# Optimization experiments

Measured on AMD Instinct MI355X. Metric: run time of the kernel, lower is better.

Reference implementation:

```python
import jax, jax.numpy as jnp
import numpy as np

NUM_CHANNEL_TYPES = 32  # global channel vocabulary (matches fill_max of channel_idx)


def setup_inputs() -> dict:
    key = jax.random.key(0)
    k1, k2, k3, k4, k5, k6 = jax.random.split(key, 6)
    B, C, H, W, E, P = 32, 8, 224, 224, 768, 16
    return {
        "x": jax.random.normal(k1, (B, C, H, W), dtype=jnp.float32),
        "channel_idx": jax.random.randint(k2, (B, C), 0, NUM_CHANNEL_TYPES, dtype=jnp.int64),
        "proj_w": jax.random.normal(k3, (E, P, P), dtype=jnp.float32) * 0.02,
        "proj_b": jax.random.normal(k4, (E,), dtype=jnp.float32) * 0.02,
        "ctx_w": jax.random.normal(k5, (E, E), dtype=jnp.float32) * 0.02,
        "ctx_b": jax.random.normal(k6, (E,), dtype=jnp.float32) * 0.02,
    }


def reference(x, channel_idx, proj_w, proj_b, ctx_w, ctx_b):
    B, C, H, W = x.shape
    E, P, _ = proj_w.shape
    Hp, Wp = H // P, W // P

    # Conv3d(1, E, kernel=(1,P,P), stride=(1,P,P)) == per-channel 2D patchify matmul
    xp = x.reshape(B, C, Hp, P, Wp, P)
    emb = jnp.einsum('bchpwq,epq->bechw', xp, proj_w) + proj_b[None, :, None, None, None]
    # emb: (B, E, C, Hp, Wp)

    # per-(sample, channel) average patch embedding -> (B, C, E)
    av_patch = emb.mean(axis=(3, 4)).transpose(0, 2, 1)
    flat = av_patch.reshape(B * C, E)
    seg = channel_idx.reshape(-1)

    # segment-mean over the batch by channel index (fused scatter-mean)
    sums = jax.ops.segment_sum(flat, seg, num_segments=NUM_CHANNEL_TYPES)
    cnt = jax.ops.segment_sum(jnp.ones((B * C,), flat.dtype), seg, num_segments=NUM_CHANNEL_TYPES)
    means = sums / jnp.maximum(cnt, 1.0)[:, None]
    chan_embed = means[seg].reshape(B, C, E)  # torch computes this under no_grad

    # context projection and broadcast-add back onto patch embeddings
    ctx = chan_embed @ ctx_w.T + ctx_b            # (B, C, E)
    out = emb + ctx.transpose(0, 2, 1)[:, :, :, None, None]

    # flatten(2).transpose(1, 2): (B, C*Hp*Wp, E)
    return out.reshape(B, E, C * Hp * Wp).transpose(0, 2, 1)
```

## Files before the change

kernel.cpp:

```cpp
#include <hip/hip_runtime.h>
#include <hip/hip_bf16.h>

typedef __attribute__((ext_vector_type(8))) short s16x8;
typedef __attribute__((ext_vector_type(4))) float f32x4;
typedef __attribute__((ext_vector_type(8))) unsigned short u16x8;
typedef __attribute__((ext_vector_type(4))) unsigned short u16x4;

static __device__ __forceinline__ unsigned short f2bf(float f) {
  unsigned int u = __float_as_uint(f);
  unsigned int r = u + 0x7fffu + ((u >> 16) & 1u);
  return (unsigned short)(r >> 16);
}
static __device__ __forceinline__ float bf2f(unsigned short s) {
  return __uint_as_float(((unsigned int)s) << 16);
}

static __device__ __forceinline__ void gload16(const void* g, void* l) {
  __builtin_amdgcn_global_load_lds(
      (const __attribute__((address_space(1))) unsigned int*)g,
      (__attribute__((address_space(3))) unsigned int*)l, 16, 0, 0);
}


__global__ void k_cvt(const float* __restrict__ in, unsigned short* __restrict__ o) {
  int i = blockIdx.x * 256 + threadIdx.x;
  float4 v = reinterpret_cast<const float4*>(in)[i];
  u16x4 pk = { f2bf(v.x), f2bf(v.y), f2bf(v.z), f2bf(v.w) };
  reinterpret_cast<u16x4*>(o)[i] = pk;
}

__global__ void k_transpose768(const float* __restrict__ in, float* __restrict__ out) {
  __shared__ float tile[32][33];
  int bx = blockIdx.x % 24, by = blockIdx.x / 24;
  int tx = threadIdx.x & 31, ty = threadIdx.x >> 5;
#pragma unroll
  for (int k = 0; k < 4; ++k)
    tile[ty + 8 * k][tx] = in[(size_t)(by * 32 + ty + 8 * k) * 768 + bx * 32 + tx];
  __syncthreads();
#pragma unroll
  for (int k = 0; k < 4; ++k)
    out[(size_t)(bx * 32 + ty + 8 * k) * 768 + by * 32 + tx] = tile[tx][ty + 8 * k];
}

__global__ __launch_bounds__(256) void k_prep(const float* __restrict__ x,
                                              unsigned short* __restrict__ xbf,
                                              float* __restrict__ avg3) {
  __shared__ __align__(16) unsigned short strip[14 * 256];
  int b = blockIdx.x;
  int bc = b / 14, hp = b - bc * 14;
  int t = threadIdx.x;
  const float* img = x + ((size_t)bc * 224 + hp * 16) * 224;

  for (int idx = t; idx < 896; idx += 256) {
    int row = idx / 56, c4 = idx - row * 56;
    float4 v = reinterpret_cast<const float4*>(img + (size_t)row * 224)[c4];
    int wp = c4 >> 2, q0 = (c4 & 3) << 2;
    u16x4 pk = { f2bf(v.x), f2bf(v.y), f2bf(v.z), f2bf(v.w) };
    *(u16x4*)&strip[wp * 256 + row * 16 + q0] = pk;
  }
  __syncthreads();

  float acc = 0.f;
#pragma unroll
  for (int wp = 0; wp < 14; ++wp) acc += bf2f(strip[wp * 256 + t]);
  avg3[((size_t)bc * 14 + hp) * 256 + t] = acc;

  const u16x8* so = (const u16x8*)strip;
  u16x8* go = (u16x8*)(xbf + ((size_t)bc * 196 + hp * 14) * 256);
  for (int i = t; i < 448; i += 256) go[i] = so[i];
}

__global__ __launch_bounds__(256) void k_segmean(const float* __restrict__ avg3,
                                                 const int* __restrict__ seg,
                                                 float* __restrict__ sp) {
  __shared__ float red[4][64];
  __shared__ int rcnt[4];
  __shared__ int ssg[256];
  int s = blockIdx.x & 31, kc = blockIdx.x >> 5;
  int t = threadIdx.x;
  int kl = t & 63, slice = t >> 6;
  int k = kc * 64 + kl;
  ssg[t] = seg[t];
  __syncthreads();
  float sum = 0.f; int cnt = 0;
  for (int bc = slice * 64; bc < slice * 64 + 64; ++bc) {
    if (ssg[bc] == s) {
      ++cnt;
      const float* row = avg3 + (size_t)bc * 14 * 256 + k;
#pragma unroll
      for (int hp = 0; hp < 14; ++hp) sum += row[hp * 256];
    }
  }
  red[slice][kl] = sum;
  if (kl == 0) rcnt[slice] = cnt;
  __syncthreads();
  if (t < 64) {
    float tot = red[0][t] + red[1][t] + red[2][t] + red[3][t];
    int c = rcnt[0] + rcnt[1] + rcnt[2] + rcnt[3];
    sp[s * 256 + kc * 64 + t] = tot / (196.0f * (float)(c > 0 ? c : 1));
  }
}

__global__ __launch_bounds__(256) void k_means2(const float* __restrict__ sp,
                                                const float* __restrict__ pw,
                                                const float* __restrict__ pb,
                                                float* __restrict__ means) {
  __shared__ float ssp[256];
  __shared__ float red[8][32];
  int s = blockIdx.x & 31, e0 = (blockIdx.x >> 5) << 5;
  int t = threadIdx.x;
  int e = t & 31, ksl = t >> 5;
  ssp[t] = sp[s * 256 + t];
  __syncthreads();
  const float4* w = reinterpret_cast<const float4*>(pw + (size_t)(e0 + e) * 256 + ksl * 32);
  float a = 0.f;
#pragma unroll
  for (int j = 0; j < 8; ++j) {
    float4 v = w[j];
    int kb = ksl * 32 + j * 4;
    a += v.x * ssp[kb] + v.y * ssp[kb + 1] + v.z * ssp[kb + 2] + v.w * ssp[kb + 3];
  }
  red[ksl][e] = a;
  __syncthreads();
  if (t < 32) {
    float tot = 0.f;
#pragma unroll
    for (int j = 0; j < 8; ++j) tot += red[j][t];
    means[s * 768 + e0 + t] = tot + pb[e0 + t];
  }
}

__global__ __launch_bounds__(256) void k_ctx2(const float* __restrict__ means,
                                              const float* __restrict__ cwT,
                                              const float* __restrict__ cb,
                                              const float* __restrict__ pb,
                                              float* __restrict__ addv) {
  __shared__ float mn[768];
  __shared__ float red[8][32];
  int s = blockIdx.x & 31, e0 = (blockIdx.x >> 5) << 5;
  int t = threadIdx.x;
  int e = t & 31, fsl = t >> 5;
  mn[t] = means[s * 768 + t];
  mn[t + 256] = means[s * 768 + 256 + t];
  mn[t + 512] = means[s * 768 + 512 + t];
  __syncthreads();
  const float* col = cwT + (size_t)fsl * 96 * 768 + e0 + e;
  float a = 0.f;
#pragma unroll 8
  for (int j = 0; j < 96; ++j) a += mn[fsl * 96 + j] * col[(size_t)j * 768];
  red[fsl][e] = a;
  __syncthreads();
  if (t < 32) {
    float tot = 0.f;
#pragma unroll
    for (int j = 0; j < 8; ++j) tot += red[j][t];
    addv[s * 768 + e0 + t] = tot + cb[e0 + t] + pb[e0 + t];
  }
}

__global__ __launch_bounds__(256) void k_gemm(
    const unsigned short* __restrict__ xbf, const unsigned short* __restrict__ wbf,
    const float* __restrict__ addv, const int* __restrict__ seg,
    float* __restrict__ out) {
  __shared__ __align__(16) unsigned short Al[128 * 64];
  __shared__ __align__(16) unsigned short Bl[128 * 64];

  int bid = blockIdx.x;
  int xcd = bid & 7, local = bid >> 3;
  int mb = xcd * 49 + local / 6;
  int nb = local - (local / 6) * 6;
  int m0 = mb << 7, n0 = nb << 7;

  int t = threadIdx.x;
  int wave = t >> 6, lane = t & 63;
  int wm = (wave >> 1) << 6, wn = (wave & 1) << 6;
  int lr = lane & 15, hi = lane >> 4;
  int axor = (lr & 7) << 4;

  int swz = (((lane & 7) ^ ((lane >> 3) & 7)) << 4);
  const char* abase = (const char*)xbf + (size_t)(m0 + (lane >> 3)) * 512 + swz + (size_t)wave * 16384;
  const char* bbase = (const char*)wbf + (size_t)(n0 + (lane >> 3)) * 512 + swz + (size_t)wave * 16384;
  char* adst = (char*)Al + wave * 4096;
  char* bdst = (char*)Bl + wave * 4096;
  const char* Alc = (const char*)Al;
  const char* Blc = (const char*)Bl;

  f32x4 acc[4][4] = {};

  for (int kt = 0; kt < 4; ++kt) {
#pragma unroll
    for (int i = 0; i < 4; ++i) {
      gload16(abase + kt * 128 + i * 4096, adst + i * 1024);
      gload16(bbase + kt * 128 + i * 4096, bdst + i * 1024);
    }
    __syncthreads();
#pragma unroll
    for (int kk = 0; kk < 2; ++kk) {
      s16x8 af[4], bv[4];
      int koff = kk * 64 + hi * 16;
#pragma unroll
      for (int i = 0; i < 4; ++i)
        af[i] = *(const s16x8*)(Alc + (wm + i * 16 + lr) * 128 + (koff ^ axor));
#pragma unroll
      for (int j = 0; j < 4; ++j)
        bv[j] = *(const s16x8*)(Blc + (wn + j * 16 + lr) * 128 + (koff ^ axor));
#pragma unroll
      for (int i = 0; i < 4; ++i)
#pragma unroll
        for (int j = 0; j < 4; ++j)
          acc[i][j] = __builtin_amdgcn_mfma_f32_16x16x32_bf16(af[i], bv[j], acc[i][j], 0, 0, 0);
    }
    __syncthreads();
  }

#pragma unroll
  for (int i = 0; i < 4; ++i) {
    int mloc = m0 + wm + i * 16 + (hi << 2);
#pragma unroll
    for (int r = 0; r < 4; ++r) {
      int M = mloc + r;
      int sgi = seg[M / 196];
      const float* av = addv + (size_t)sgi * 768 + n0 + wn + lr;
      float* orow = out + (size_t)M * 768 + n0 + wn + lr;
#pragma unroll
      for (int j = 0; j < 4; ++j)
        orow[j * 16] = acc[i][j][r] + av[j * 16];
    }
  }
}

__global__ void k_avgpatch_fb(const float* __restrict__ x, float* __restrict__ avg) {
  int bc = blockIdx.x;
  int k = threadIdx.x;
  int p = k >> 4, q = k & 15;
  const float* base = x + (size_t)bc * 224 * 224;
  float s = 0.f;
  for (int hp = 0; hp < 14; ++hp) {
    const float* row = base + (hp * 16 + p) * 224 + q;
#pragma unroll
    for (int wp = 0; wp < 14; ++wp) s += row[wp * 16];
  }
  avg[bc * 256 + k] = s * (1.0f / 196.0f);
}

__global__ __launch_bounds__(768) void k_chain_fb(const float* __restrict__ avg,
                                                  const int* __restrict__ seg,
                                                  const float* __restrict__ pw,
                                                  const float* __restrict__ pb,
                                                  const float* __restrict__ cwT,
                                                  const float* __restrict__ cb,
                                                  float* __restrict__ addv) {
  __shared__ float sp[256];
  __shared__ float mn[768];
  __shared__ int ssg[256];
  int s = blockIdx.x, t = threadIdx.x;
  if (t < 256) ssg[t] = seg[t];
  __syncthreads();
  if (t < 256) {
    float sum = 0.f; int c = 0;
    for (int bc = 0; bc < 256; ++bc)
      if (ssg[bc] == s) { sum += avg[bc * 256 + t]; ++c; }
    sp[t] = sum / (float)(c > 0 ? c : 1);
  }
  __syncthreads();
  {
    const float4* w = reinterpret_cast<const float4*>(pw + (size_t)t * 256);
    float a = 0.f;
#pragma unroll 8
    for (int k = 0; k < 64; ++k) {
      float4 v = w[k];
      a += v.x * sp[k * 4] + v.y * sp[k * 4 + 1] + v.z * sp[k * 4 + 2] + v.w * sp[k * 4 + 3];
    }
    mn[t] = a + pb[t];
  }
  __syncthreads();
  float a2 = 0.f;
#pragma unroll 8
  for (int f = 0; f < 768; ++f) a2 += mn[f] * cwT[(size_t)f * 768 + t];
  addv[s * 768 + t] = a2 + cb[t] + pb[t];
}

__global__ __launch_bounds__(256) void k_gemm_fb(
    const float* __restrict__ x, const unsigned short* __restrict__ wbf,
    const float* __restrict__ addv, const int* __restrict__ seg,
    float* __restrict__ out) {
  __shared__ unsigned short Al[128][40];
  __shared__ unsigned short Bl[128][40];
  int bid = blockIdx.x;
  int xcd = bid & 7, local = bid >> 3;
  int mb = xcd * 49 + local / 6;
  int nb = local - (local / 6) * 6;
  int m0 = mb << 7, n0 = nb << 7;
  int t = threadIdx.x;
  int wave = t >> 6, lane = t & 63;
  int wm = (wave >> 1) << 6, wn = (wave & 1) << 6;
  int lr = lane & 15, lk = (lane >> 4) << 3;
  int mstage = m0 + (t >> 1);
  int halfA = t & 1;
  int bc = mstage / 196;
  int pij = mstage - bc * 196;
  int hp = pij / 14;
  int wp = pij - hp * 14;
  const float* xbase = x + ((size_t)bc * 224 + hp * 16 + halfA) * 224 + wp * 16;
  const unsigned short* bsrc = wbf + (size_t)(n0 + (t >> 1)) * 256 + halfA * 16;
  unsigned short* adst = &Al[t >> 1][halfA * 16];
  unsigned short* bdst = &Bl[t >> 1][halfA * 16];
  f32x4 acc[4][4] = {};
  for (int ks = 0; ks < 8; ++ks) {
    __syncthreads();
    *(u16x8*)bdst       = *(const u16x8*)(bsrc + ks * 32);
    *(u16x8*)(bdst + 8) = *(const u16x8*)(bsrc + ks * 32 + 8);
    {
      const float4* src = reinterpret_cast<const float4*>(xbase + ks * 448);
      float4 v0 = src[0], v1 = src[1], v2 = src[2], v3 = src[3];
      u16x8 p0 = { f2bf(v0.x), f2bf(v0.y), f2bf(v0.z), f2bf(v0.w),
                   f2bf(v1.x), f2bf(v1.y), f2bf(v1.z), f2bf(v1.w) };
      u16x8 p1 = { f2bf(v2.x), f2bf(v2.y), f2bf(v2.z), f2bf(v2.w),
                   f2bf(v3.x), f2bf(v3.y), f2bf(v3.z), f2bf(v3.w) };
      *(u16x8*)adst = p0;
      *(u16x8*)(adst + 8) = p1;
    }
    __syncthreads();
    s16x8 af[4], bfv[4];
#pragma unroll
    for (int i = 0; i < 4; ++i) af[i] = *(const s16x8*)&Al[wm + i * 16 + lr][lk];
#pragma unroll
    for (int j = 0; j < 4; ++j) bfv[j] = *(const s16x8*)&Bl[wn + j * 16 + lr][lk];
#pragma unroll
    for (int i = 0; i < 4; ++i)
#pragma unroll
      for (int j = 0; j < 4; ++j)
        acc[i][j] = __builtin_amdgcn_mfma_f32_16x16x32_bf16(af[i], bfv[j], acc[i][j], 0, 0, 0);
  }
#pragma unroll
  for (int i = 0; i < 4; ++i) {
    int mloc = m0 + wm + i * 16 + ((lane >> 4) << 2);
#pragma unroll
    for (int r = 0; r < 4; ++r) {
      int M = mloc + r;
      int sgi = seg[M / 196];
      const float* av = addv + (size_t)sgi * 768 + n0 + wn + lr;
      float* orow = out + (size_t)M * 768 + n0 + wn + lr;
#pragma unroll
      for (int j = 0; j < 4; ++j)
        orow[j * 16] = acc[i][j][r] + av[j * 16];
    }
  }
}


extern "C" void kernel_launch(void* const* d_in, const int* in_sizes, int n_in,
                              void* d_out, int out_size, void* d_ws, size_t ws_size,
                              hipStream_t stream) {
  (void)in_sizes; (void)n_in; (void)out_size;
  const float* x  = (const float*)d_in[0];
  const int*   sg = (const int*)d_in[1];
  const float* pw = (const float*)d_in[2];
  const float* pb = (const float*)d_in[3];
  const float* cw = (const float*)d_in[4];
  const float* cb = (const float*)d_in[5];
  float* out = (float*)d_out;

  char* ws = (char*)d_ws;
  unsigned short* pwbf = (unsigned short*)ws;
  float* cwT   = (float*)(ws + 393216);
  float* addv  = (float*)(ws + 2752512);
  float* sp    = (float*)(ws + 2850816);
  float* means = (float*)(ws + 2883584);
  float* avg3  = (float*)(ws + 2981888);
  unsigned short* xbf = (unsigned short*)(ws + 6651904);
  const size_t NEED = 6651904u + 25690112u;

  k_cvt<<<192, 256, 0, stream>>>(pw, pwbf);
  k_transpose768<<<576, 256, 0, stream>>>(cw, cwT);
  if (ws_size >= NEED) {
    k_prep<<<3584, 256, 0, stream>>>(x, xbf, avg3);
    k_segmean<<<128, 256, 0, stream>>>(avg3, sg, sp);
    k_means2<<<768, 256, 0, stream>>>(sp, pw, pb, means);
    k_ctx2<<<768, 256, 0, stream>>>(means, cwT, cb, pb, addv);
    k_gemm<<<2352, 256, 0, stream>>>(xbf, pwbf, addv, sg, out);
  } else {
    float* avgp = (float*)(ws + 2981888);
    k_avgpatch_fb<<<256, 256, 0, stream>>>(x, avgp);
    k_chain_fb<<<32, 768, 0, stream>>>(avgp, sg, pw, pb, cwT, cb, addv);
    k_gemm_fb<<<2352, 256, 0, stream>>>(x, pwbf, addv, sg, out);
  }
}
```

Before: 101.6 us.

## Merge prep kernels into one launch and vectorize GEMM epilogue stores via swapped MFMA operands

Folds the weight bf16 conversion and the ctx_w transpose into the x-prep kernel as extra block ranges, cutting two kernel launches and their serialization. It also swaps the MFMA A/B operands so each lane holds four consecutive output columns. That lets the epilogue do 16-byte vector loads of the add vector and 16-byte stores of the output instead of scalar strided stores. The output write is the dominant memory traffic, so wider stores should improve write coalescing.

```diff
diff --git a/kernel.cpp b/kernel.cpp
--- a/kernel.cpp
+++ b/kernel.cpp
@@ -21,53 +21,52 @@
       (__attribute__((address_space(3))) unsigned int*)l, 16, 0, 0);
 }
 
-
-__global__ void k_cvt(const float* __restrict__ in, unsigned short* __restrict__ o) {
-  int i = blockIdx.x * 256 + threadIdx.x;
-  float4 v = reinterpret_cast<const float4*>(in)[i];
-  u16x4 pk = { f2bf(v.x), f2bf(v.y), f2bf(v.z), f2bf(v.w) };
-  reinterpret_cast<u16x4*>(o)[i] = pk;
-}
-
-__global__ void k_transpose768(const float* __restrict__ in, float* __restrict__ out) {
-  __shared__ float tile[32][33];
-  int bx = blockIdx.x % 24, by = blockIdx.x / 24;
-  int tx = threadIdx.x & 31, ty = threadIdx.x >> 5;
-#pragma unroll
-  for (int k = 0; k < 4; ++k)
-    tile[ty + 8 * k][tx] = in[(size_t)(by * 32 + ty + 8 * k) * 768 + bx * 32 + tx];
-  __syncthreads();
-#pragma unroll
-  for (int k = 0; k < 4; ++k)
-    out[(size_t)(bx * 32 + ty + 8 * k) * 768 + by * 32 + tx] = tile[tx][ty + 8 * k];
-}
-
-__global__ __launch_bounds__(256) void k_prep(const float* __restrict__ x,
+__global__ __launch_bounds__(256) void k_mega(const float* __restrict__ x,
                                               unsigned short* __restrict__ xbf,
-                                              float* __restrict__ avg3) {
-  __shared__ __align__(16) unsigned short strip[14 * 256];
-  int b = blockIdx.x;
-  int bc = b / 14, hp = b - bc * 14;
-  int t = threadIdx.x;
-  const float* img = x + ((size_t)bc * 224 + hp * 16) * 224;
-
-  for (int idx = t; idx < 896; idx += 256) {
-    int row = idx / 56, c4 = idx - row * 56;
-    float4 v = reinterpret_cast<const float4*>(img + (size_t)row * 224)[c4];
-    int wp = c4 >> 2, q0 = (c4 & 3) << 2;
+                                              float* __restrict__ avg3,
+                                              const float* __restrict__ pw,
+                                              unsigned short* __restrict__ pwbf,
+                                              const float* __restrict__ cw,
+                                              float* __restrict__ cwT) {
+  __shared__ __align__(16) char smem[7168];
+  int b = blockIdx.x, t = threadIdx.x;
+  if (b < 3584) {
+    unsigned short* strip = (unsigned short*)smem;
+    int bc = b / 14, hp = b - bc * 14;
+    const float* img = x + ((size_t)bc * 224 + hp * 16) * 224;
+    for (int idx = t; idx < 896; idx += 256) {
+      int row = idx / 56, c4 = idx - row * 56;
+      float4 v = reinterpret_cast<const float4*>(img + (size_t)row * 224)[c4];
+      int wp = c4 >> 2, q0 = (c4 & 3) << 2;
+      u16x4 pk = { f2bf(v.x), f2bf(v.y), f2bf(v.z), f2bf(v.w) };
+      *(u16x4*)&strip[wp * 256 + row * 16 + q0] = pk;
+    }
+    __syncthreads();
+    float acc = 0.f;
+#pragma unroll
+    for (int wp = 0; wp < 14; ++wp) acc += bf2f(strip[wp * 256 + t]);
+    avg3[((size_t)bc * 14 + hp) * 256 + t] = acc;
+    const u16x8* so = (const u16x8*)strip;
+    u16x8* go = (u16x8*)(xbf + ((size_t)bc * 196 + hp * 14) * 256);
+    for (int i = t; i < 448; i += 256) go[i] = so[i];
+  } else if (b < 3776) {
+    int i = (b - 3584) * 256 + t;
+    float4 v = reinterpret_cast<const float4*>(pw)[i];
     u16x4 pk = { f2bf(v.x), f2bf(v.y), f2bf(v.z), f2bf(v.w) };
-    *(u16x4*)&strip[wp * 256 + row * 16 + q0] = pk;
-  }
-  __syncthreads();
-
-  float acc = 0.f;
-#pragma unroll
-  for (int wp = 0; wp < 14; ++wp) acc += bf2f(strip[wp * 256 + t]);
-  avg3[((size_t)bc * 14 + hp) * 256 + t] = acc;
-
-  const u16x8* so = (const u16x8*)strip;
-  u16x8* go = (u16x8*)(xbf + ((size_t)bc * 196 + hp * 14) * 256);
-  for (int i = t; i < 448; i += 256) go[i] = so[i];
+    reinterpret_cast<u16x4*>(pwbf)[i] = pk;
+  } else {
+    float (*tile)[33] = (float(*)[33])smem;
+    int bid2 = b - 3776;
+    int bx = bid2 % 24, by = bid2 / 24;
+    int tx = t & 31, ty = t >> 5;
+#pragma unroll
+    for (int k = 0; k < 4; ++k)
+      tile[ty + 8 * k][tx] = cw[(size_t)(by * 32 + ty + 8 * k) * 768 + bx * 32 + tx];
+    __syncthreads();
+#pragma unroll
+    for (int k = 0; k < 4; ++k)
+      cwT[(size_t)(bx * 32 + ty + 8 * k) * 768 + by * 32 + tx] = tile[tx][ty + 8 * k];
+  }
 }
 
 __global__ __launch_bounds__(256) void k_segmean(const float* __restrict__ avg3,
@@ -208,25 +207,45 @@
       for (int i = 0; i < 4; ++i)
 #pragma unroll
         for (int j = 0; j < 4; ++j)
-          acc[i][j] = __builtin_amdgcn_mfma_f32_16x16x32_bf16(af[i], bv[j], acc[i][j], 0, 0, 0);
+          acc[i][j] = __builtin_amdgcn_mfma_f32_16x16x32_bf16(bv[j], af[i], acc[i][j], 0, 0, 0);
     }
     __syncthreads();
   }
 
 #pragma unroll
   for (int i = 0; i < 4; ++i) {
-    int mloc = m0 + wm + i * 16 + (hi << 2);
-#pragma unroll
-    for (int r = 0; r < 4; ++r) {
-      int M = mloc + r;
-      int sgi = seg[M / 196];
-      const float* av = addv + (size_t)sgi * 768 + n0 + wn + lr;
-      float* orow = out + (size_t)M * 768 + n0 + wn + lr;
-#pragma unroll
-      for (int j = 0; j < 4; ++j)
-        orow[j * 16] = acc[i][j][r] + av[j * 16];
-    }
-  }
+    int M = m0 + wm + i * 16 + lr;
+    int sgi = seg[M / 196];
+    const float* av = addv + (size_t)sgi * 768 + n0 + wn + hi * 4;
+    float* orow = out + (size_t)M * 768 + n0 + wn + hi * 4;
+#pragma unroll
+    for (int j = 0; j < 4; ++j) {
+      f32x4 a4 = *(const f32x4*)(av + j * 16);
+      f32x4 v = acc[i][j];
+      v.x += a4.x; v.y += a4.y; v.z += a4.z; v.w += a4.w;
+      *(f32x4*)(orow + j * 16) = v;
+    }
+  }
+}
+
+__global__ void k_cvt_fb(const float* __restrict__ in, unsigned short* __restrict__ o) {
+  int i = blockIdx.x * 256 + threadIdx.x;
+  float4 v = reinterpret_cast<const float4*>(in)[i];
+  u16x4 pk = { f2bf(v.x), f2bf(v.y), f2bf(v.z), f2bf(v.w) };
+  reinterpret_cast<u16x4*>(o)[i] = pk;
+}
+
+__global__ void k_transpose_fb(const float* __restrict__ in, float* __restrict__ out) {
+  __shared__ float tile[32][33];
+  int bx = blockIdx.x % 24, by = blockIdx.x / 24;
+  int tx = threadIdx.x & 31, ty = threadIdx.x >> 5;
+#pragma unroll
+  for (int k = 0; k < 4; ++k)
+    tile[ty + 8 * k][tx] = in[(size_t)(by * 32 + ty + 8 * k) * 768 + bx * 32 + tx];
+  __syncthreads();
+#pragma unroll
+  for (int k = 0; k < 4; ++k)
+    out[(size_t)(bx * 32 + ty + 8 * k) * 768 + by * 32 + tx] = tile[tx][ty + 8 * k];
 }
 
 __global__ void k_avgpatch_fb(const float* __restrict__ x, float* __restrict__ avg) {
@@ -330,20 +349,21 @@
     for (int i = 0; i < 4; ++i)
 #pragma unroll
       for (int j = 0; j < 4; ++j)
-        acc[i][j] = __builtin_amdgcn_mfma_f32_16x16x32_bf16(af[i], bfv[j], acc[i][j], 0, 0, 0);
+        acc[i][j] = __builtin_amdgcn_mfma_f32_16x16x32_bf16(bfv[j], af[i], acc[i][j], 0, 0, 0);
   }
 #pragma unroll
   for (int i = 0; i < 4; ++i) {
-    int mloc = m0 + wm + i * 16 + ((lane >> 4) << 2);
-#pragma unroll
-    for (int r = 0; r < 4; ++r) {
-      int M = mloc + r;
-      int sgi = seg[M / 196];
-      const float* av = addv + (size_t)sgi * 768 + n0 + wn + lr;
-      float* orow = out + (size_t)M * 768 + n0 + wn + lr;
-#pragma unroll
-      for (int j = 0; j < 4; ++j)
-        orow[j * 16] = acc[i][j][r] + av[j * 16];
+    int M = m0 + wm + i * 16 + lr;
+    int sgi = seg[M / 196];
+    int hi = lane >> 4;
+    const float* av = addv + (size_t)sgi * 768 + n0 + wn + hi * 4;
+    float* orow = out + (size_t)M * 768 + n0 + wn + hi * 4;
+#pragma unroll
+    for (int j = 0; j < 4; ++j) {
+      f32x4 a4 = *(const f32x4*)(av + j * 16);
+      f32x4 v = acc[i][j];
+      v.x += a4.x; v.y += a4.y; v.z += a4.z; v.w += a4.w;
+      *(f32x4*)(orow + j * 16) = v;
     }
   }
 }
@@ -371,16 +391,16 @@
   unsigned short* xbf = (unsigned short*)(ws + 6651904);
   const size_t NEED = 6651904u + 25690112u;
 
-  k_cvt<<<192, 256, 0, stream>>>(pw, pwbf);
-  k_transpose768<<<576, 256, 0, stream>>>(cw, cwT);
   if (ws_size >= NEED) {
-    k_prep<<<3584, 256, 0, stream>>>(x, xbf, avg3);
+    k_mega<<<4352, 256, 0, stream>>>(x, xbf, avg3, pw, pwbf, cw, cwT);
     k_segmean<<<128, 256, 0, stream>>>(avg3, sg, sp);
     k_means2<<<768, 256, 0, stream>>>(sp, pw, pb, means);
     k_ctx2<<<768, 256, 0, stream>>>(means, cwT, cb, pb, addv);
     k_gemm<<<2352, 256, 0, stream>>>(xbf, pwbf, addv, sg, out);
   } else {
     float* avgp = (float*)(ws + 2981888);
+    k_cvt_fb<<<192, 256, 0, stream>>>(pw, pwbf);
+    k_transpose_fb<<<576, 256, 0, stream>>>(cw, cwT);
     k_avgpatch_fb<<<256, 256, 0, stream>>>(x, avgp);
     k_chain_fb<<<32, 768, 0, stream>>>(avgp, sg, pw, pb, cwT, cb, addv);
     k_gemm_fb<<<2352, 256, 0, stream>>>(x, pwbf, addv, sg, out);
```

Result: faster. 87.86 us (-13.5%).
